# Kernel tuning notes

Measured on AMD Instinct MI355X. Metric: run time of the kernel, lower is better.

## Reference

```python
import jax, jax.numpy as jnp
import numpy as np

NH, D, MULT, NLAYER = 8, 512, 32, 3
N_INT = D * MULT // NH  # 2048 sparse-code dim per head
EPS = 1e-5
THETA = 2.0 ** 16
NUM_CLASSES = 2


def _ln(x):
    # LayerNorm over last dim, no affine (elementwise_affine=False), biased var
    m = jnp.mean(x, axis=-1, keepdims=True)
    v = jnp.mean((x - m) ** 2, axis=-1, keepdims=True)
    return (x - m) * jax.lax.rsqrt(v + EPS)


def _rotate_half(x):
    x1, x2 = jnp.split(x, 2, axis=-1)
    return jnp.concatenate((-x2, x1), axis=-1)


def _attn(Qs, V):
    # Qs: [B,nh,T,N] ReLU-sparse codes (Q == K), V: [B,1,T,D] raw hidden
    T = Qs.shape[2]
    half = 1.0 / (THETA ** (jnp.arange(0, N_INT, 2, dtype=jnp.float32) / N_INT))
    freqs = jnp.concatenate((half, half))                      # [N]
    ph = jnp.arange(T, dtype=jnp.float32)[:, None] * freqs[None, :]  # [T,N]
    QR = Qs * jnp.cos(ph) + _rotate_half(Qs) * jnp.sin(ph)
    scores = jnp.einsum('bhtn,bhsn->bhts', QR, QR)             # no softmax, no scaling
    mask = jnp.tril(jnp.ones((T, T), dtype=scores.dtype), k=-1)  # strictly causal
    scores = scores * mask
    return jnp.einsum('bhts,bsd->bhtd', scores, V[:, 0])       # [B,nh,T,D]


def setup_inputs():
    key = jax.random.key(0)
    ks = jax.random.split(key, 8)
    B, T, NA, F = 2, 1024, 93, 4
    in_dim, out_dim = NA * F, NA * NUM_CLASSES
    s = 0.02
    return dict(
        x=jax.random.normal(ks[0], (B, T, NA, F), dtype=jnp.float32),
        Wi=jax.random.normal(ks[1], (in_dim, D), dtype=jnp.float32) * s,
        bi=jnp.zeros((D,), jnp.float32),
        enc=jax.random.uniform(ks[2], (NH, D, N_INT), jnp.float32, -s, s),
        enc_v=jax.random.uniform(ks[3], (NH, D, N_INT), jnp.float32, -s, s),
        dec=jax.random.uniform(ks[4], (NH * N_INT, D), jnp.float32, -s, s),
        Wo=jax.random.normal(ks[5], (D, out_dim), dtype=jnp.float32) * s,
        bo=jnp.zeros((out_dim,), jnp.float32),
    )


def reference(x, Wi, bi, enc, enc_v, dec, Wo, bo):
    B, T, NA, F = x.shape
    h = _ln((x.reshape(B, T, NA * F) @ Wi + bi)[:, None])      # [B,1,T,D]
    for _ in range(NLAYER):
        h_res = h
        h_sp = jax.nn.relu(jnp.einsum('bxtd,hdn->bhtn', h, enc))      # [B,nh,T,N]
        yKV = _ln(_attn(h_sp, h))                                     # [B,nh,T,D]
        y_sp = jax.nn.relu(jnp.einsum('bhtd,hdn->bhtn', yKV, enc_v))  # [B,nh,T,N]
        xy = h_sp * y_sp                                              # gating
        # transpose(1,2).reshape(B,1,T,nh*N): head-major flatten of codes
        xy_flat = xy.transpose(0, 2, 1, 3).reshape(B, 1, T, NH * N_INT)
        h = _ln(h_res + _ln(xy_flat @ dec))                           # [B,1,T,D]
    out = h[:, 0] @ Wo + bo                                           # [B,T,NA*C]
    return out.reshape(B, T, NA, NUM_CLASSES)
```

## Files before the change

### kernel.cpp

```cpp
#include <hip/hip_runtime.h>

typedef __bf16 bf16;
typedef __attribute__((ext_vector_type(8))) __bf16 bf16x8;
typedef __attribute__((ext_vector_type(4))) float f32x4;
typedef __attribute__((ext_vector_type(2))) _Float16 h16x2;

#define T_SEQ 1024
#define D_MODEL 512
#define N_INT 2048
#define NHEADS 8
#define IN_DIM 372
#define IN_PAD 384
#define OUT_DIM 186
#define OUT_PAD 256

__device__ inline void gld16(const bf16* g, bf16* l) {
  __builtin_amdgcn_global_load_lds((const __attribute__((address_space(1))) void*)g,
                                   (__attribute__((address_space(3))) void*)l, 16, 0, 0);
}

__device__ inline void block_sum2(float& a, float& b, float* red) {
#pragma unroll
  for (int o = 32; o > 0; o >>= 1) {
    a += __shfl_down(a, o, 64);
    b += __shfl_down(b, o, 64);
  }
  __syncthreads();
  if ((threadIdx.x & 63) == 0) {
    int w = threadIdx.x >> 6;
    red[2 * w] = a;
    red[2 * w + 1] = b;
  }
  __syncthreads();
  a = red[0] + red[2] + red[4] + red[6];
  b = red[1] + red[3] + red[5] + red[7];
}

__global__ __launch_bounds__(256) void transpose_cvt(const float* __restrict__ in,
                                                     bf16* __restrict__ out,
                                                     int rows, int cols) {
  __shared__ float tile[32][33];
  size_t zoff = (size_t)blockIdx.z * rows * cols;
  in += zoff;
  out += zoff;
  int c0 = blockIdx.x * 32, r0 = blockIdx.y * 32;
#pragma unroll
  for (int i = threadIdx.y; i < 32; i += 8)
    tile[i][threadIdx.x] = in[(size_t)(r0 + i) * cols + c0 + threadIdx.x];
  __syncthreads();
#pragma unroll
  for (int i = threadIdx.y; i < 32; i += 8)
    out[(size_t)(c0 + i) * rows + r0 + threadIdx.x] = (bf16)tile[threadIdx.x][i];
}

__global__ __launch_bounds__(256) void pad_trans(const float* __restrict__ in,
                                                 bf16* __restrict__ out,
                                                 int R, int C, int outLd) {
  __shared__ float tile[32][33];
  int c0 = blockIdx.x * 32, r0 = blockIdx.y * 32;
#pragma unroll
  for (int i = threadIdx.y; i < 32; i += 8) {
    int r = r0 + i, c = c0 + threadIdx.x;
    tile[i][threadIdx.x] = (r < R && c < C) ? in[(size_t)r * C + c] : 0.f;
  }
  __syncthreads();
#pragma unroll
  for (int i = threadIdx.y; i < 32; i += 8)
    out[(size_t)(c0 + i) * outLd + r0 + threadIdx.x] = (bf16)tile[threadIdx.x][i];
}

__global__ __launch_bounds__(256) void cvt_pad_x(const float* __restrict__ x,
                                                 bf16* __restrict__ xbf) {
  size_t r = blockIdx.x;
  for (int c = threadIdx.x; c < IN_PAD; c += 256)
    xbf[r * IN_PAD + c] = (c < IN_DIM) ? (bf16)x[r * IN_DIM + c] : (bf16)0.f;
}

__global__ __launch_bounds__(256) void rope_tables(h16x2* __restrict__ cs) {
  int t = blockIdx.x;
  for (int i = threadIdx.x; i < 1024; i += 256) {
    float ph = (float)t * exp2f(-16.0f * (float)i * (1.0f / 1024.0f));
    h16x2 v;
    v[0] = (_Float16)cosf(ph);
    v[1] = (_Float16)sinf(ph);
    cs[(size_t)t * 1024 + i] = v;
  }
}

__global__ __launch_bounds__(256) void ln0(const float* __restrict__ zin,
                                           float* __restrict__ h, bf16* __restrict__ hbf,
                                           bf16* __restrict__ hT) {
  __shared__ float red[8];
  size_t r = blockIdx.x;
  int tid = threadIdx.x;
  float v0 = zin[r * 512 + tid], v1 = zin[r * 512 + tid + 256];
  float s = v0 + v1, s2 = v0 * v0 + v1 * v1;
  block_sum2(s, s2, red);
  float mean = s * (1.f / 512.f);
  float var = s2 * (1.f / 512.f) - mean * mean;
  float rs = rsqrtf(var + 1e-5f);
  float o0 = (v0 - mean) * rs, o1 = (v1 - mean) * rs;
  h[r * 512 + tid] = o0;
  h[r * 512 + tid + 256] = o1;
  hbf[r * 512 + tid] = (bf16)o0;
  hbf[r * 512 + tid + 256] = (bf16)o1;
  int b = (int)(r >> 10), t = (int)(r & (T_SEQ - 1));
  hT[((size_t)b * 512 + tid) * T_SEQ + t] = (bf16)o0;
  hT[((size_t)b * 512 + tid + 256) * T_SEQ + t] = (bf16)o1;
}

__global__ __launch_bounds__(256) void ln_rows(bf16* __restrict__ io) {
  const int wid = threadIdx.x >> 6, lane = threadIdx.x & 63;
  size_t r = (size_t)blockIdx.x * 4 + wid;
  bf16* p = io + r * 512 + lane * 8;
  bf16x8 v = *(const bf16x8*)p;
  float f[8], s = 0.f, s2 = 0.f;
#pragma unroll
  for (int j = 0; j < 8; ++j) {
    f[j] = (float)v[j];
    s += f[j];
    s2 += f[j] * f[j];
  }
#pragma unroll
  for (int o = 32; o > 0; o >>= 1) {
    s += __shfl_xor(s, o, 64);
    s2 += __shfl_xor(s2, o, 64);
  }
  float mean = s * (1.f / 512.f);
  float var = s2 * (1.f / 512.f) - mean * mean;
  float rs = rsqrtf(var + 1e-5f);
  bf16x8 o;
#pragma unroll
  for (int j = 0; j < 8; ++j) o[j] = (bf16)((f[j] - mean) * rs);
  *(bf16x8*)p = o;
}

__global__ __launch_bounds__(256) void psum_lnd(const bf16* __restrict__ part,
                                                float* __restrict__ h, bf16* __restrict__ hbf,
                                                bf16* __restrict__ hT) {
  __shared__ float red[8];
  int b = blockIdx.x >> 10;
  int r = blockIdx.x & 1023;
  int tid = threadIdx.x;
  float z0 = 0.f, z1 = 0.f;
#pragma unroll
  for (int k = 0; k < 16; ++k) {
    size_t off = ((size_t)(b * 16 + k) << 19) + (size_t)r * 512;
    z0 += (float)part[off + tid];
    z1 += (float)part[off + tid + 256];
  }
  float s = z0 + z1, s2 = z0 * z0 + z1 * z1;
  block_sum2(s, s2, red);
  float m1 = s * (1.f / 512.f);
  float v1_ = s2 * (1.f / 512.f) - m1 * m1;
  float rs1 = rsqrtf(v1_ + 1e-5f);
  size_t R = (size_t)b * T_SEQ + r;
  float a0 = (z0 - m1) * rs1 + h[R * 512 + tid];
  float a1 = (z1 - m1) * rs1 + h[R * 512 + tid + 256];
  s = a0 + a1;
  s2 = a0 * a0 + a1 * a1;
  block_sum2(s, s2, red);
  float m2 = s * (1.f / 512.f);
  float v2_ = s2 * (1.f / 512.f) - m2 * m2;
  float rs2 = rsqrtf(v2_ + 1e-5f);
  float o0 = (a0 - m2) * rs2, o1 = (a1 - m2) * rs2;
  h[R * 512 + tid] = o0;
  h[R * 512 + tid + 256] = o1;
  hbf[R * 512 + tid] = (bf16)o0;
  hbf[R * 512 + tid + 256] = (bf16)o1;
  hT[((size_t)b * 512 + tid) * T_SEQ + r] = (bf16)o0;
  hT[((size_t)b * 512 + tid + 256) * T_SEQ + r] = (bf16)o1;
}

template <int MODE, int TN>
__device__ __forceinline__ void gemm_body(const bf16* __restrict__ Abase,
                                          const bf16* __restrict__ Bbase,
                                          const bf16* __restrict__ aux,
                                          const float* __restrict__ fbias,
                                          float* __restrict__ fout,
                                          bf16* __restrict__ bout) {
  const int id = blockIdx.x;
  int zz = 0, r_, cb = 0;
  if constexpr (MODE >= 5) {
    r_ = id;
  } else if constexpr (MODE == 4) {
    cb = id & 31;
    r_ = id >> 5;
  } else {
    zz = id & 15;
    r_ = id >> 4;
  }
  int bi, bj;
  if constexpr (MODE == 1) {
    int l = r_;
    bi = (int)sqrtf((float)l);
    while ((bi + 1) * (bi + 2) <= l) ++bi;
    while (bi * (bi + 1) > l) --bi;
    bj = l - bi * (bi + 1);
  } else if constexpr (MODE >= 5) {
    bi = r_ & 15;
    bj = r_ >> 4;
  } else {
    bi = r_ & 7;
    bj = r_ >> 3;
  }

  const bf16* A;
  const bf16* Bt;
  int lda, ldb, kend;
  if constexpr (MODE == 1) {
    A = Abase + ((size_t)zz << 21); lda = N_INT;
    Bt = A; ldb = N_INT;
    kend = N_INT;
  } else if constexpr (MODE == 2) {
    A = Abase + ((size_t)zz << 20); lda = T_SEQ;
    Bt = Bbase + (size_t)(zz >> 3) * 512 * T_SEQ; ldb = T_SEQ;
    kend = (bi + 1) * 128;
  } else if constexpr (MODE == 3) {
    A = Abase + ((size_t)zz << 19); lda = 512;
    Bt = Bbase + (size_t)(zz & 7) * N_INT * 512; ldb = 512;
    kend = 512;
  } else if constexpr (MODE == 4) {
    A = Abase + ((size_t)(cb >> 4) << 24) + (size_t)(cb & 15) * 1024; lda = 16384;
    Bt = Bbase + (size_t)(cb & 15) * 1024; ldb = 16384;
    kend = 1024;
  } else if constexpr (MODE == 5) {
    A = Abase; lda = IN_PAD;
    Bt = Bbase; ldb = IN_PAD;
    kend = IN_PAD;
  } else {
    A = Abase; lda = 512;
    Bt = Bbase; ldb = 512;
    kend = 512;
  }

  const int tid = threadIdx.x;
  const int trow = tid >> 3, tq = tid & 7;
  const int sq = tq ^ (trow & 7);
  const bf16* ags = A + (size_t)(bi * 128 + trow) * lda + sq * 8;
  const bf16* bgs = Bt + (size_t)(bj * TN + trow) * ldb + sq * 8;

  __shared__ __align__(16) bf16 As[2][128 * 64];
  __shared__ __align__(16) bf16 Bs[2][TN * 64];
  const int so = tid * 8;

  const int lane = tid & 63, wid = tid >> 6;
  const int wr = wid >> 1, wc = wid & 1;
  const int fr = lane & 15, fg = lane >> 4;
  const int axor = fr & 7;
  constexpr int NR = TN / 32;

  f32x4 acc[4][NR] = {};

  auto stage = [&](int buf, int kk) {
#pragma unroll
    for (int p = 0; p < 4; ++p)
      gld16(ags + (size_t)(p * 32) * lda + kk, &As[buf][p * 2048 + so]);
#pragma unroll
    for (int p = 0; p < TN / 32; ++p)
      gld16(bgs + (size_t)(p * 32) * ldb + kk, &Bs[buf][p * 2048 + so]);
  };

  const int nt = kend >> 6;
  stage(0, 0);
  asm volatile("s_waitcnt vmcnt(0)" ::: "memory");
  __builtin_amdgcn_s_barrier();

  for (int t = 0; t < nt; ++t) {
    const int cur = t & 1;
    if (t + 1 < nt) stage(cur ^ 1, (t + 1) << 6);

    __builtin_amdgcn_s_setprio(1);
#pragma unroll
    for (int s = 0; s < 2; ++s) {
      bf16x8 af[4], bfv[NR];
#pragma unroll
      for (int m = 0; m < 4; ++m)
        af[m] = *(const bf16x8*)(&As[cur][(wr * 64 + m * 16 + fr) * 64 + (((s * 4 + fg) ^ axor) * 8)]);
#pragma unroll
      for (int n = 0; n < NR; ++n)
        bfv[n] = *(const bf16x8*)(&Bs[cur][(wc * (TN / 2) + n * 16 + fr) * 64 + (((s * 4 + fg) ^ axor) * 8)]);
#pragma unroll
      for (int m = 0; m < 4; ++m)
#pragma unroll
        for (int n = 0; n < NR; ++n)
          acc[m][n] = __builtin_amdgcn_mfma_f32_16x16x32_bf16(af[m], bfv[n], acc[m][n], 0, 0, 0);
    }
    __builtin_amdgcn_s_setprio(0);

    asm volatile("s_waitcnt vmcnt(0)" ::: "memory");
    __builtin_amdgcn_sched_barrier(0);
    __builtin_amdgcn_s_barrier();
    __builtin_amdgcn_sched_barrier(0);
  }

  if constexpr (MODE >= 5) {
#pragma unroll
    for (int m = 0; m < 4; ++m) {
#pragma unroll
      for (int n = 0; n < NR; ++n) {
        int c = bj * TN + wc * (TN / 2) + n * 16 + fr;
#pragma unroll
        for (int j = 0; j < 4; ++j) {
          int r = bi * 128 + wr * 64 + m * 16 + fg * 4 + j;
          float v = acc[m][n][j];
          if constexpr (MODE == 5) {
            fout[(size_t)r * 512 + c] = v + fbias[c];
          } else {
            if (c < OUT_DIM) fout[(size_t)r * OUT_DIM + c] = v + fbias[c];
          }
        }
      }
    }
  } else {
    bf16* stg = &As[0][0];
#pragma unroll
    for (int m = 0; m < 4; ++m)
#pragma unroll
      for (int n = 0; n < NR; ++n) {
        int lc = wc * (TN / 2) + n * 16 + fr;
#pragma unroll
        for (int j = 0; j < 4; ++j) {
          int lr = wr * 64 + m * 16 + fg * 4 + j;
          float v = acc[m][n][j];
          if constexpr (MODE == 3) v = fmaxf(v, 0.f);
          stg[lr * TN + lc] = (bf16)v;
        }
      }
    __syncthreads();
    constexpr int TPR = TN / 8;
    constexpr int RSTEP = 256 / TPR;
    const int c8 = (tid % TPR) * 8;
    const int lr0 = tid / TPR;
#pragma unroll
    for (int lr = lr0; lr < 128; lr += RSTEP) {
      bf16x8 v = *(const bf16x8*)&stg[lr * TN + c8];
      int r = bi * 128 + lr;
      int c = bj * TN + c8;
      if constexpr (MODE == 1) {
        bf16x8 o;
#pragma unroll
        for (int k = 0; k < 8; ++k) o[k] = (c + k < r) ? v[k] : (bf16)0.f;
        *(bf16x8*)&bout[((size_t)zz << 20) + (size_t)r * T_SEQ + c] = o;
      } else if constexpr (MODE == 2) {
        *(bf16x8*)&bout[((size_t)zz << 19) + (size_t)r * 512 + c] = v;
      } else if constexpr (MODE == 3) {
        bf16x8 g = *(const bf16x8*)&aux[((size_t)zz << 21) + (size_t)r * N_INT + c];
        bf16x8 o;
#pragma unroll
        for (int k = 0; k < 8; ++k) o[k] = (bf16)((float)v[k] * (float)g[k]);
        *(bf16x8*)&bout[((size_t)(zz >> 3) << 24) + (size_t)r * 16384 + (size_t)(zz & 7) * N_INT + c] = o;
      } else {
        *(bf16x8*)&bout[((size_t)cb << 19) + (size_t)r * 512 + c] = v;
      }
    }
  }
}

__global__ __launch_bounds__(256, 3) void g_scores(const bf16* A, bf16* o) {
  gemm_body<1, 64>(A, nullptr, nullptr, nullptr, nullptr, o);
}
__global__ __launch_bounds__(256, 3) void g_pv(const bf16* A, const bf16* B, bf16* o) {
  gemm_body<2, 64>(A, B, nullptr, nullptr, nullptr, o);
}
__global__ __launch_bounds__(256, 2) void g_gate(const bf16* A, const bf16* B, const bf16* aux, bf16* o) {
  gemm_body<3, 128>(A, B, aux, nullptr, nullptr, o);
}
__global__ __launch_bounds__(256, 2) void g_dec(const bf16* A, const bf16* B, bf16* o) {
  gemm_body<4, 128>(A, B, nullptr, nullptr, nullptr, o);
}
__global__ __launch_bounds__(256, 2) void g_in(const bf16* A, const bf16* B, const float* bias, float* o) {
  gemm_body<5, 128>(A, B, nullptr, bias, o, nullptr);
}
__global__ __launch_bounds__(256, 2) void g_out(const bf16* A, const bf16* B, const float* bias, float* o) {
  gemm_body<6, 128>(A, B, nullptr, bias, o, nullptr);
}

__global__ __launch_bounds__(256, 2) void g_hspr(const bf16* __restrict__ hbf,
                                                 const bf16* __restrict__ encT,
                                                 const h16x2* __restrict__ cs,
                                                 bf16* __restrict__ hsp,
                                                 bf16* __restrict__ qr) {
  const int id = blockIdx.x;
  const int zz = id & 15;
  const int r_ = id >> 4;
  const int bi = r_ & 7;
  const int bj = r_ >> 3;

  const bf16* B0 = encT + (size_t)(zz & 7) * N_INT * 512 + (size_t)(bj * 64) * 512;
  const bf16* B1 = B0 + (size_t)1024 * 512;
  const bf16* hbf_b = hbf + (size_t)(zz >> 3) * T_SEQ * 512;

  const int tid = threadIdx.x;
  const int trow = tid >> 3, tq = tid & 7;
  const int sq = tq ^ (trow & 7);
  const bf16* ags = hbf_b + (size_t)(bi * 128 + trow) * 512 + sq * 8;
  const bf16* bgs0 = B0 + (size_t)trow * 512 + sq * 8;
  const bf16* bgs1 = B1 + (size_t)trow * 512 + sq * 8;

  __shared__ __align__(16) bf16 As[2][128 * 64];
  __shared__ __align__(16) bf16 Bs[2][2 * 64 * 64];
  const int so = tid * 8;

  const int lane = tid & 63, wid = tid >> 6;
  const int wr = wid >> 1, wc = wid & 1;
  const int fr = lane & 15, fg = lane >> 4;
  const int axor = fr & 7;

  f32x4 acc[4][2][2] = {};

  auto stage = [&](int buf, int kk) {
#pragma unroll
    for (int p = 0; p < 4; ++p)
      gld16(ags + (size_t)(p * 32) * 512 + kk, &As[buf][p * 2048 + so]);
    gld16(bgs0 + kk, &Bs[buf][0 * 2048 + so]);
    gld16(bgs0 + (size_t)32 * 512 + kk, &Bs[buf][1 * 2048 + so]);
    gld16(bgs1 + kk, &Bs[buf][2 * 2048 + so]);
    gld16(bgs1 + (size_t)32 * 512 + kk, &Bs[buf][3 * 2048 + so]);
  };

  stage(0, 0);
  asm volatile("s_waitcnt vmcnt(0)" ::: "memory");
  __builtin_amdgcn_s_barrier();

  for (int t = 0; t < 8; ++t) {
    const int cur = t & 1;
    if (t + 1 < 8) stage(cur ^ 1, (t + 1) << 6);

    __builtin_amdgcn_s_setprio(1);
#pragma unroll
    for (int s = 0; s < 2; ++s) {
      bf16x8 af[4], bfv[2][2];
#pragma unroll
      for (int m = 0; m < 4; ++m)
        af[m] = *(const bf16x8*)(&As[cur][(wr * 64 + m * 16 + fr) * 64 + (((s * 4 + fg) ^ axor) * 8)]);
#pragma unroll
      for (int pp = 0; pp < 2; ++pp)
#pragma unroll
        for (int n = 0; n < 2; ++n)
          bfv[pp][n] = *(const bf16x8*)(&Bs[cur][pp * 4096 + (wc * 32 + n * 16 + fr) * 64 + (((s * 4 + fg) ^ axor) * 8)]);
#pragma unroll
      for (int m = 0; m < 4; ++m)
#pragma unroll
        for (int n = 0; n < 2; ++n)
#pragma unroll
          for (int pp = 0; pp < 2; ++pp)
            acc[m][n][pp] = __builtin_amdgcn_mfma_f32_16x16x32_bf16(af[m], bfv[pp][n], acc[m][n][pp], 0, 0, 0);
    }
    __builtin_amdgcn_s_setprio(0);

    asm volatile("s_waitcnt vmcnt(0)" ::: "memory");
    __builtin_amdgcn_sched_barrier(0);
    __builtin_amdgcn_s_barrier();
    __builtin_amdgcn_sched_barrier(0);
  }

  bf16* sL = &As[0][0];
  bf16* sH = &As[1][0];
#pragma unroll
  for (int m = 0; m < 4; ++m)
#pragma unroll
    for (int n = 0; n < 2; ++n) {
      int lc = wc * 32 + n * 16 + fr;
#pragma unroll
      for (int j = 0; j < 4; ++j) {
        int lr = wr * 64 + m * 16 + fg * 4 + j;
        sL[lr * 64 + lc] = (bf16)fmaxf(acc[m][n][0][j], 0.f);
        sH[lr * 64 + lc] = (bf16)fmaxf(acc[m][n][1][j], 0.f);
      }
    }
  __syncthreads();

  const size_t hb = (size_t)zz * T_SEQ;
  const int c8 = (tid & 7) * 8;
  const int lr0 = tid >> 3;
#pragma unroll
  for (int lr = lr0; lr < 128; lr += 32) {
    int r = bi * 128 + lr;
    int c = bj * 64 + c8;
    bf16x8 lo = *(const bf16x8*)&sL[lr * 64 + c8];
    bf16x8 hi = *(const bf16x8*)&sH[lr * 64 + c8];
    size_t base = (hb + r) * N_INT + c;
    *(bf16x8*)&hsp[base] = lo;
    *(bf16x8*)&hsp[base + 1024] = hi;
    const h16x2* csp = &cs[(size_t)r * 1024 + c];
    bf16x8 qlo, qhi;
#pragma unroll
    for (int k = 0; k < 8; ++k) {
      h16x2 p = csp[k];
      float co = (float)p[0], si = (float)p[1];
      float v0 = (float)lo[k], v1 = (float)hi[k];
      qlo[k] = (bf16)(v0 * co - v1 * si);
      qhi[k] = (bf16)(v1 * co + v0 * si);
    }
    *(bf16x8*)&qr[base] = qlo;
    *(bf16x8*)&qr[base + 1024] = qhi;
  }
}

extern "C" void kernel_launch(void* const* d_in, const int* in_sizes, int n_in,
                              void* d_out, int out_size, void* d_ws, size_t ws_size,
                              hipStream_t stream) {
  const float* x = (const float*)d_in[0];
  const float* Wi = (const float*)d_in[1];
  const float* bi = (const float*)d_in[2];
  const float* enc = (const float*)d_in[3];
  const float* encv = (const float*)d_in[4];
  const float* dec = (const float*)d_in[5];
  const float* Wo = (const float*)d_in[6];
  const float* bo = (const float*)d_in[7];
  float* out = (float*)d_out;

  const size_t NEED = 253000000;
  if (ws_size < NEED) return;

  char* w = (char*)d_ws;
  auto alloc = [&](size_t bytes) {
    char* p = w;
    w += (bytes + 255) & ~(size_t)255;
    return p;
  };
  bf16* encT = (bf16*)alloc((size_t)NHEADS * N_INT * 512 * 2);
  bf16* encvT = (bf16*)alloc((size_t)NHEADS * N_INT * 512 * 2);
  bf16* decT = (bf16*)alloc((size_t)512 * 16384 * 2);
  h16x2* cs = (h16x2*)alloc((size_t)T_SEQ * 1024 * 4);
  float* h = (float*)alloc((size_t)2048 * 512 * 4);
  bf16* hbf = (bf16*)alloc((size_t)2048 * 512 * 2);
  bf16* hT = (bf16*)alloc((size_t)2048 * 512 * 2);
  bf16* hsp = (bf16*)alloc((size_t)2 * NHEADS * T_SEQ * N_INT * 2);
  bf16* qr = (bf16*)alloc((size_t)2 * NHEADS * T_SEQ * N_INT * 2);
  bf16* S = (bf16*)alloc((size_t)2 * NHEADS * T_SEQ * T_SEQ * 2);
  bf16* ykv = (bf16*)alloc((size_t)2 * NHEADS * T_SEQ * 512 * 2);
  float* zbuf = (float*)alloc((size_t)2048 * 512 * 4);
  bf16* WoT = (bf16*)alloc((size_t)OUT_PAD * 512 * 2);
  bf16* xbf = S;
  bf16* WiT = S + 1048576;

  transpose_cvt<<<dim3(64, 16, 8), dim3(32, 8), 0, stream>>>(enc, encT, 512, N_INT);
  transpose_cvt<<<dim3(64, 16, 8), dim3(32, 8), 0, stream>>>(encv, encvT, 512, N_INT);
  transpose_cvt<<<dim3(16, 512, 1), dim3(32, 8), 0, stream>>>(dec, decT, 16384, 512);
  pad_trans<<<dim3(16, 12), dim3(32, 8), 0, stream>>>(Wi, WiT, IN_DIM, 512, IN_PAD);
  pad_trans<<<dim3(8, 16), dim3(32, 8), 0, stream>>>(Wo, WoT, 512, OUT_DIM, 512);
  cvt_pad_x<<<2048, 256, 0, stream>>>(x, xbf);
  rope_tables<<<1024, 256, 0, stream>>>(cs);
  g_in<<<64, 256, 0, stream>>>(xbf, WiT, bi, zbuf);
  ln0<<<2048, 256, 0, stream>>>(zbuf, h, hbf, hT);

  for (int L = 0; L < 3; ++L) {
    g_hspr<<<2048, 256, 0, stream>>>(hbf, encT, cs, hsp, qr);
    g_scores<<<1152, 256, 0, stream>>>(qr, S);
    g_pv<<<1024, 256, 0, stream>>>(S, hT, ykv);
    ln_rows<<<4096, 256, 0, stream>>>(ykv);
    g_gate<<<2048, 256, 0, stream>>>(ykv, encvT, hsp, qr);
    g_dec<<<1024, 256, 0, stream>>>(qr, decT, S);
    psum_lnd<<<2048, 256, 0, stream>>>(S, h, hbf, hT);
  }
  g_out<<<32, 256, 0, stream>>>(hbf, WoT, bo, out);
}
```

Measured before the change: 865.3 us.

## Triple-buffer gate GEMM and halve split-K partitions in decoder GEMM

Adds a PIPE template parameter so the gate GEMM uses three shared-memory stages, with vmcnt-based waits that keep two tiles in flight, and relaxes its launch-bounds occupancy hint. It also changes the decoder GEMM's split-K from 16 slices of 1024 to 8 slices of 2048. That halves its grid and the partial buffers the reduction kernel must read. The cost is more LDS per block for the gate kernel, which may reduce occupancy, and fewer but longer blocks for the decoder GEMM.

```diff
diff --git a/kernel.cpp b/kernel.cpp
--- a/kernel.cpp
+++ b/kernel.cpp
@@ -144,8 +144,8 @@
   int tid = threadIdx.x;
   float z0 = 0.f, z1 = 0.f;
 #pragma unroll
-  for (int k = 0; k < 16; ++k) {
-    size_t off = ((size_t)(b * 16 + k) << 19) + (size_t)r * 512;
+  for (int k = 0; k < 8; ++k) {
+    size_t off = ((size_t)(b * 8 + k) << 19) + (size_t)r * 512;
     z0 += (float)part[off + tid];
     z1 += (float)part[off + tid + 256];
   }
@@ -172,7 +172,7 @@
   hT[((size_t)b * 512 + tid + 256) * T_SEQ + r] = (bf16)o1;
 }
 
-template <int MODE, int TN>
+template <int MODE, int TN, int PIPE>
 __device__ __forceinline__ void gemm_body(const bf16* __restrict__ Abase,
                                           const bf16* __restrict__ Bbase,
                                           const bf16* __restrict__ aux,
@@ -184,8 +184,8 @@
   if constexpr (MODE >= 5) {
     r_ = id;
   } else if constexpr (MODE == 4) {
-    cb = id & 31;
-    r_ = id >> 5;
+    cb = id & 15;
+    r_ = id >> 4;
   } else {
     zz = id & 15;
     r_ = id >> 4;
@@ -221,9 +221,9 @@
     Bt = Bbase + (size_t)(zz & 7) * N_INT * 512; ldb = 512;
     kend = 512;
   } else if constexpr (MODE == 4) {
-    A = Abase + ((size_t)(cb >> 4) << 24) + (size_t)(cb & 15) * 1024; lda = 16384;
-    Bt = Bbase + (size_t)(cb & 15) * 1024; ldb = 16384;
-    kend = 1024;
+    A = Abase + ((size_t)(cb >> 3) << 24) + (size_t)(cb & 7) * 2048; lda = 16384;
+    Bt = Bbase + (size_t)(cb & 7) * 2048; ldb = 16384;
+    kend = 2048;
   } else if constexpr (MODE == 5) {
     A = Abase; lda = IN_PAD;
     Bt = Bbase; ldb = IN_PAD;
@@ -240,8 +240,9 @@
   const bf16* ags = A + (size_t)(bi * 128 + trow) * lda + sq * 8;
   const bf16* bgs = Bt + (size_t)(bj * TN + trow) * ldb + sq * 8;
 
-  __shared__ __align__(16) bf16 As[2][128 * 64];
-  __shared__ __align__(16) bf16 Bs[2][TN * 64];
+  constexpr int NBUF = PIPE + 1;
+  __shared__ __align__(16) bf16 As[NBUF][128 * 64];
+  __shared__ __align__(16) bf16 Bs[NBUF][TN * 64];
   const int so = tid * 8;
 
   const int lane = tid & 63, wid = tid >> 6;
@@ -261,15 +262,7 @@
       gld16(bgs + (size_t)(p * 32) * ldb + kk, &Bs[buf][p * 2048 + so]);
   };
 
-  const int nt = kend >> 6;
-  stage(0, 0);
-  asm volatile("s_waitcnt vmcnt(0)" ::: "memory");
-  __builtin_amdgcn_s_barrier();
-
-  for (int t = 0; t < nt; ++t) {
-    const int cur = t & 1;
-    if (t + 1 < nt) stage(cur ^ 1, (t + 1) << 6);
-
+  auto compute = [&](int cur) {
     __builtin_amdgcn_s_setprio(1);
 #pragma unroll
     for (int s = 0; s < 2; ++s) {
@@ -287,11 +280,41 @@
           acc[m][n] = __builtin_amdgcn_mfma_f32_16x16x32_bf16(af[m], bfv[n], acc[m][n], 0, 0, 0);
     }
     __builtin_amdgcn_s_setprio(0);
-
+  };
+
+  const int nt = kend >> 6;
+  if constexpr (PIPE == 1) {
+    stage(0, 0);
     asm volatile("s_waitcnt vmcnt(0)" ::: "memory");
-    __builtin_amdgcn_sched_barrier(0);
     __builtin_amdgcn_s_barrier();
-    __builtin_amdgcn_sched_barrier(0);
+    for (int t = 0; t < nt; ++t) {
+      const int cur = t & 1;
+      if (t + 1 < nt) stage(cur ^ 1, (t + 1) << 6);
+      compute(cur);
+      asm volatile("s_waitcnt vmcnt(0)" ::: "memory");
+      __builtin_amdgcn_sched_barrier(0);
+      __builtin_amdgcn_s_barrier();
+      __builtin_amdgcn_sched_barrier(0);
+    }
+  } else {
+    stage(0, 0);
+    if (nt > 1) stage(1, 64);
+    if (nt > 1) asm volatile("s_waitcnt vmcnt(8)" ::: "memory");
+    else asm volatile("s_waitcnt vmcnt(0)" ::: "memory");
+    __builtin_amdgcn_s_barrier();
+    for (int t = 0; t < nt; ++t) {
+      const int cur = t % 3;
+      if (t + 2 < nt) stage((t + 2) % 3, (t + 2) << 6);
+      compute(cur);
+      if (t + 1 < nt) {
+        if (t + 2 < nt) asm volatile("s_waitcnt vmcnt(8)" ::: "memory");
+        else asm volatile("s_waitcnt vmcnt(0)" ::: "memory");
+        __builtin_amdgcn_sched_barrier(0);
+        __builtin_amdgcn_s_barrier();
+        __builtin_amdgcn_sched_barrier(0);
+      }
+    }
+    __syncthreads();
   }
 
   if constexpr (MODE >= 5) {
@@ -358,22 +381,22 @@
 }
 
 __global__ __launch_bounds__(256, 3) void g_scores(const bf16* A, bf16* o) {
-  gemm_body<1, 64>(A, nullptr, nullptr, nullptr, nullptr, o);
+  gemm_body<1, 64, 1>(A, nullptr, nullptr, nullptr, nullptr, o);
 }
 __global__ __launch_bounds__(256, 3) void g_pv(const bf16* A, const bf16* B, bf16* o) {
-  gemm_body<2, 64>(A, B, nullptr, nullptr, nullptr, o);
-}
-__global__ __launch_bounds__(256, 2) void g_gate(const bf16* A, const bf16* B, const bf16* aux, bf16* o) {
-  gemm_body<3, 128>(A, B, aux, nullptr, nullptr, o);
+  gemm_body<2, 64, 1>(A, B, nullptr, nullptr, nullptr, o);
+}
+__global__ __launch_bounds__(256) void g_gate(const bf16* A, const bf16* B, const bf16* aux, bf16* o) {
+  gemm_body<3, 128, 2>(A, B, aux, nullptr, nullptr, o);
 }
 __global__ __launch_bounds__(256, 2) void g_dec(const bf16* A, const bf16* B, bf16* o) {
-  gemm_body<4, 128>(A, B, nullptr, nullptr, nullptr, o);
+  gemm_body<4, 128, 1>(A, B, nullptr, nullptr, nullptr, o);
 }
 __global__ __launch_bounds__(256, 2) void g_in(const bf16* A, const bf16* B, const float* bias, float* o) {
-  gemm_body<5, 128>(A, B, nullptr, bias, o, nullptr);
+  gemm_body<5, 128, 1>(A, B, nullptr, bias, o, nullptr);
 }
 __global__ __launch_bounds__(256, 2) void g_out(const bf16* A, const bf16* B, const float* bias, float* o) {
-  gemm_body<6, 128>(A, B, nullptr, bias, o, nullptr);
+  gemm_body<6, 128, 1>(A, B, nullptr, bias, o, nullptr);
 }
 
 __global__ __launch_bounds__(256, 2) void g_hspr(const bf16* __restrict__ hbf,
@@ -552,7 +575,7 @@
     g_pv<<<1024, 256, 0, stream>>>(S, hT, ykv);
     ln_rows<<<4096, 256, 0, stream>>>(ykv);
     g_gate<<<2048, 256, 0, stream>>>(ykv, encvT, hsp, qr);
-    g_dec<<<1024, 256, 0, stream>>>(qr, decT, S);
+    g_dec<<<512, 256, 0, stream>>>(qr, decT, S);
     psum_lnd<<<2048, 256, 0, stream>>>(S, h, hbf, hT);
   }
   g_out<<<32, 256, 0, stream>>>(hbf, WoT, bo, out);
```

After: 923.5 us. +6.7%, slower.
